# Kernel tuning notes

Measured on AMD Instinct MI355X. Metric: run time of the kernel, lower is better.

Reference implementation:

```python
import jax, jax.numpy as jnp
import numpy as np

C = 64
B, H, W = 4, 64, 64


def setup_inputs() -> dict:
    key = jax.random.key(0)
    ks = jax.random.split(key, 8)
    s = 0.05
    x = jax.random.normal(ks[0], (B, C, H, W), dtype=jnp.float32)
    Wq = jax.random.normal(ks[1], (C // 4, C), dtype=jnp.float32) * s
    bq = jax.random.normal(ks[2], (C // 4,), dtype=jnp.float32) * s
    Wk = jax.random.normal(ks[3], (C // 4, C), dtype=jnp.float32) * s
    bk = jax.random.normal(ks[4], (C // 4,), dtype=jnp.float32) * s
    Wv = jax.random.normal(ks[5], (C, C), dtype=jnp.float32) * s
    bv = jax.random.normal(ks[6], (C,), dtype=jnp.float32) * s
    gamma = jax.random.normal(ks[7], (1,), dtype=jnp.float32)
    return {"x": x, "Wq": Wq, "bq": bq, "Wk": Wk, "bk": bk, "Wv": Wv, "bv": bv, "gamma": gamma}


def reference(x, Wq, bq, Wk, bk, Wv, bv, gamma):
    b, c, h, w = x.shape
    n = h * w
    xf = x.reshape(b, c, n)  # [B, C, N]
    # 1x1 convs == channel GEMMs
    q = jnp.einsum('bcn,oc->bon', xf, Wq) + bq[None, :, None]  # [B, C/4, N]
    k = jnp.einsum('bcn,oc->bon', xf, Wk) + bk[None, :, None]  # [B, C/4, N]
    v = jnp.einsum('bcn,oc->bon', xf, Wv) + bv[None, :, None]  # [B, C, N]
    # attention[b, i, j] over key positions j (no 1/sqrt(d) scaling, per source)
    scores = jnp.einsum('bci,bcj->bij', q, k)  # [B, N, N]
    attn = jax.nn.softmax(scores, axis=-1)
    out = jnp.einsum('bcj,bij->bci', v, attn)  # [B, C, N]
    out = out.reshape(b, c, h, w)
    return gamma * out + x
```

## Files before the change

### kernel.cpp

```cpp
#include <hip/hip_runtime.h>

typedef short short8  __attribute__((ext_vector_type(8)));
typedef short short4v __attribute__((ext_vector_type(4)));
typedef float f32x4   __attribute__((ext_vector_type(4)));

static __device__ __forceinline__ unsigned short f2bf(float f) {
  unsigned int u = __builtin_bit_cast(unsigned int, f);
  u += 0x7fffu + ((u >> 16) & 1u);
  return (unsigned short)(u >> 16);
}
static __device__ __forceinline__ float bf2f(unsigned short u) {
  unsigned int v = ((unsigned int)u) << 16;
  return __builtin_bit_cast(float, v);
}
static __device__ __forceinline__ unsigned int pack2bf_rtz(float lo, float hi) {
  return __builtin_amdgcn_perm(__builtin_bit_cast(unsigned int, hi),
                               __builtin_bit_cast(unsigned int, lo), 0x07060302u);
}

__global__ __launch_bounds__(256) void qkv_mfma(
    const float* __restrict__ x,
    const float* __restrict__ Wq, const float* __restrict__ bq,
    const float* __restrict__ Wk, const float* __restrict__ bk,
    const float* __restrict__ Wv, const float* __restrict__ bv,
    unsigned short* __restrict__ qb, unsigned short* __restrict__ kb,
    unsigned short* __restrict__ vb)
{
  const int rt   = blockIdx.x;
  const int nt   = blockIdx.y;
  const int b    = blockIdx.z;
  const int lane = threadIdx.x & 63;
  const int wave = threadIdx.x >> 6;
  const int l15  = lane & 15;
  const int quad = lane >> 4;
  const int n    = nt * 64 + wave * 16 + l15;

  const float* wbase; const float* bias; int row0;
  if (rt == 0)      { wbase = Wq; bias = bq; row0 = 0; }
  else if (rt == 1) { wbase = Wk; bias = bk; row0 = 0; }
  else              { wbase = Wv; bias = bv; row0 = (rt - 2) * 16; }

  short8 bfrag[2];
#pragma unroll
  for (int ks = 0; ks < 2; ++ks)
#pragma unroll
    for (int jj = 0; jj < 8; ++jj) {
      const int c = ks * 32 + quad * 8 + jj;
      bfrag[ks][jj] = (short)f2bf(x[((size_t)(b * 64 + c)) * 4096 + n]);
    }

  short8 afrag[2];
#pragma unroll
  for (int ks = 0; ks < 2; ++ks) {
    f32x4 w0 = *(const f32x4*)(wbase + (row0 + l15) * 64 + ks * 32 + quad * 8);
    f32x4 w1 = *(const f32x4*)(wbase + (row0 + l15) * 64 + ks * 32 + quad * 8 + 4);
#pragma unroll
    for (int jj = 0; jj < 4; ++jj) {
      afrag[ks][jj]     = (short)f2bf(w0[jj]);
      afrag[ks][jj + 4] = (short)f2bf(w1[jj]);
    }
  }

  f32x4 acc;
#pragma unroll
  for (int r = 0; r < 4; ++r)
    acc[r] = bias[row0 + quad * 4 + r];
  acc = __builtin_amdgcn_mfma_f32_16x16x32_bf16(afrag[0], bfrag[0], acc, 0, 0, 0);
  acc = __builtin_amdgcn_mfma_f32_16x16x32_bf16(afrag[1], bfrag[1], acc, 0, 0, 0);

  if (rt <= 1) {
    if (rt == 0) {
#pragma unroll
      for (int r = 0; r < 4; ++r) acc[r] *= 1.44269504088896340736f;
    }
    short4v sv;
#pragma unroll
    for (int r = 0; r < 4; ++r) sv[r] = (short)f2bf(acc[r]);
    unsigned short* dst = (rt == 0 ? qb : kb);
    *(short4v*)(dst + (((size_t)b * 4096 + n) * 16) + quad * 4) = sv;
  } else {
#pragma unroll
    for (int r = 0; r < 4; ++r) {
      const int c = row0 + quad * 4 + r;
      vb[((size_t)(b * 64 + c)) * 4096 + n] = f2bf(acc[r]);
    }
  }
}

__global__ __launch_bounds__(512) void flash_fused(
    const unsigned short* __restrict__ qb, const unsigned short* __restrict__ kb,
    const unsigned short* __restrict__ vb,
    const float* __restrict__ x, const float* __restrict__ gptr,
    float* __restrict__ out)
{
  __shared__ unsigned short p_lds[8 * 4096];

  const int qg   = blockIdx.x;
  const int b    = blockIdx.y;
  const int t    = threadIdx.x;
  const int wave = t >> 6;
  const int lane = t & 63;
  const int l15  = lane & 15;
  const int quad = lane >> 4;
  const int sw   = l15 & 7;

  short8 qfrag[4];
#pragma unroll
  for (int qt = 0; qt < 4; ++qt) {
    qfrag[qt] = (short8)0;
    if (quad < 2) {
      const int iq = qg * 64 + qt * 16 + l15;
      qfrag[qt] = *(const short8*)(qb + (((size_t)b * 4096 + iq) * 16 + quad * 8));
    }
  }

  const unsigned short* vbb = vb + (size_t)b * 64 * 4096;
  const unsigned short* kbb = kb + (size_t)b * 4096 * 16;
  f32x4 acc[4][4];
#pragma unroll
  for (int qt = 0; qt < 4; ++qt)
#pragma unroll
    for (int ct = 0; ct < 4; ++ct) acc[qt][ct] = (f32x4)0.f;
  float lp[4] = {0.f, 0.f, 0.f, 0.f};
  unsigned short* pw = p_lds + wave * 4096;

  const int jbeg = wave * 512;
  const int jend = jbeg + 512;

  short8 kf[4];
#pragma unroll
  for (int sub = 0; sub < 4; ++sub) {
    kf[sub] = (short8)0;
    if (quad < 2)
      kf[sub] = *(const short8*)(kbb + (size_t)(jbeg + sub * 16 + l15) * 16 + quad * 8);
  }

#pragma unroll 1
  for (int j0 = jbeg; j0 < jend; j0 += 64) {
    short8 vf[2][4];
#pragma unroll
    for (int kc = 0; kc < 2; ++kc) {
      const int vcol = j0 + kc * 32 + quad * 8;
#pragma unroll
      for (int ct = 0; ct < 4; ++ct)
        vf[kc][ct] = *(const short8*)(vbb + (size_t)(ct * 16 + l15) * 4096 + vcol);
    }

#pragma unroll
    for (int qt = 0; qt < 4; ++qt) {
#pragma unroll
      for (int sub = 0; sub < 4; ++sub) {
        f32x4 sc = __builtin_amdgcn_mfma_f32_16x16x32_bf16(kf[sub], qfrag[qt], (f32x4)0.f, 0, 0, 0);
        float p0 = __builtin_amdgcn_exp2f(sc[0]);
        float p1 = __builtin_amdgcn_exp2f(sc[1]);
        float p2 = __builtin_amdgcn_exp2f(sc[2]);
        float p3 = __builtin_amdgcn_exp2f(sc[3]);
        lp[qt] += (p0 + p1) + (p2 + p3);
        const int ch = (sub * 2 + (quad >> 1)) ^ sw;
        unsigned int* dst = (unsigned int*)(pw + (qt * 16 + l15) * 64 + ch * 8 + (quad & 1) * 4);
        dst[0] = pack2bf_rtz(p0, p1);
        dst[1] = pack2bf_rtz(p2, p3);
      }
    }

    short8 kfn[4];
    const int jn = j0 + 64;
    const bool more = (jn < jend);
#pragma unroll
    for (int sub = 0; sub < 4; ++sub) {
      kfn[sub] = (short8)0;
      if (more && quad < 2)
        kfn[sub] = *(const short8*)(kbb + (size_t)(jn + sub * 16 + l15) * 16 + quad * 8);
    }

    __builtin_amdgcn_s_setprio(1);
#pragma unroll
    for (int kc = 0; kc < 2; ++kc) {
#pragma unroll
      for (int qt = 0; qt < 4; ++qt) {
        short8 pf = *(const short8*)(pw + (qt * 16 + l15) * 64 + ((kc * 4 + quad) ^ sw) * 8);
#pragma unroll
        for (int ct = 0; ct < 4; ++ct)
          acc[qt][ct] = __builtin_amdgcn_mfma_f32_16x16x32_bf16(vf[kc][ct], pf, acc[qt][ct], 0, 0, 0);
      }
    }
    __builtin_amdgcn_s_setprio(0);

#pragma unroll
    for (int sub = 0; sub < 4; ++sub) kf[sub] = kfn[sub];
  }

  float xr[8];
#pragma unroll
  for (int r = 0; r < 8; ++r) {
    const int c = wave * 8 + r;
    xr[r] = x[((size_t)(b * 64 + c)) * 4096 + (size_t)qg * 64 + lane];
  }

#pragma unroll
  for (int qt = 0; qt < 4; ++qt) {
    lp[qt] += __shfl_xor(lp[qt], 16);
    lp[qt] += __shfl_xor(lp[qt], 32);
  }

#pragma unroll
  for (int qt = 0; qt < 4; ++qt)
#pragma unroll
    for (int ct = 0; ct < 4; ++ct) {
      short4v sv;
#pragma unroll
      for (int r = 0; r < 4; ++r) sv[r] = (short)f2bf(acc[qt][ct][r]);
      const int q = qt * 16 + l15;
      const unsigned off = (unsigned)(q * 128 + (ct * 16 + quad * 4) * 2)
                         ^ (unsigned)((q & 7) << 4);
      *(short4v*)((char*)pw + off) = sv;
    }
  __syncthreads();

  float o[8] = {0.f, 0.f, 0.f, 0.f, 0.f, 0.f, 0.f, 0.f};
  const unsigned roff = (unsigned)(lane * 128 + wave * 16)
                      ^ (unsigned)((lane & 7) << 4);
#pragma unroll
  for (int w = 0; w < 8; ++w) {
    short8 v = *(const short8*)((const char*)(p_lds + w * 4096) + roff);
#pragma unroll
    for (int r = 0; r < 8; ++r) o[r] += bf2f((unsigned short)v[r]);
  }
  __syncthreads();

  float* lf = (float*)p_lds;
  if (lane < 16) {
#pragma unroll
    for (int qt = 0; qt < 4; ++qt)
      lf[wave * 64 + qt * 16 + lane] = lp[qt];
  }
  __syncthreads();
  float lsum = 0.f;
#pragma unroll
  for (int w = 0; w < 8; ++w) lsum += lf[w * 64 + lane];
  const float li = 1.f / lsum;
  const float g  = gptr[0];

#pragma unroll
  for (int r = 0; r < 8; ++r) {
    const int c = wave * 8 + r;
    const size_t off = ((size_t)(b * 64 + c)) * 4096 + (size_t)qg * 64 + lane;
    out[off] = g * (o[r] * li) + xr[r];
  }
}

extern "C" void kernel_launch(void* const* d_in, const int* in_sizes, int n_in,
                              void* d_out, int out_size, void* d_ws, size_t ws_size,
                              hipStream_t stream)
{
  const float* x  = (const float*)d_in[0];
  const float* Wq = (const float*)d_in[1];
  const float* bq = (const float*)d_in[2];
  const float* Wk = (const float*)d_in[3];
  const float* bk = (const float*)d_in[4];
  const float* Wv = (const float*)d_in[5];
  const float* bv = (const float*)d_in[6];
  const float* g  = (const float*)d_in[7];

  unsigned short* ws = (unsigned short*)d_ws;
  unsigned short* qb = ws;
  unsigned short* kb = ws + 262144;
  unsigned short* vb = ws + 524288;
  float* ob = (float*)d_out;

  hipLaunchKernelGGL(qkv_mfma, dim3(6, 64, 4), dim3(256), 0, stream,
                     x, Wq, bq, Wk, bk, Wv, bv, qb, kb, vb);
  hipLaunchKernelGGL(flash_fused, dim3(64, 4), dim3(512), 0, stream,
                     qb, kb, vb, x, g, ob);
}
```

Baseline: 96.07 us.

## Fuse QKV projection into attention kernel with cooperative grid sync

Merges the QKV projection kernel and the flash attention kernel into one cooperative launch. Each block computes Q for its own query tile straight into LDS, plus its share of K and V for global memory, then runs a grid-wide sync before the attention phase. This removes one kernel launch and the global round trip for Q. In exchange it adds a grid barrier and requires all 256 blocks of 512 threads with 64KB LDS to be co-resident, and the cooperative launch path may carry its own overhead.

```diff
diff --git a/kernel.cpp b/kernel.cpp
--- a/kernel.cpp
+++ b/kernel.cpp
@@ -1,4 +1,7 @@
 #include <hip/hip_runtime.h>
+#include <hip/hip_cooperative_groups.h>
+
+namespace cg = cooperative_groups;
 
 typedef short short8  __attribute__((ext_vector_type(8)));
 typedef short short4v __attribute__((ext_vector_type(4)));
@@ -18,83 +21,15 @@
                                __builtin_bit_cast(unsigned int, lo), 0x07060302u);
 }
 
-__global__ __launch_bounds__(256) void qkv_mfma(
+__global__ __launch_bounds__(512) void fused_all(
     const float* __restrict__ x,
     const float* __restrict__ Wq, const float* __restrict__ bq,
     const float* __restrict__ Wk, const float* __restrict__ bk,
     const float* __restrict__ Wv, const float* __restrict__ bv,
-    unsigned short* __restrict__ qb, unsigned short* __restrict__ kb,
-    unsigned short* __restrict__ vb)
-{
-  const int rt   = blockIdx.x;
-  const int nt   = blockIdx.y;
-  const int b    = blockIdx.z;
-  const int lane = threadIdx.x & 63;
-  const int wave = threadIdx.x >> 6;
-  const int l15  = lane & 15;
-  const int quad = lane >> 4;
-  const int n    = nt * 64 + wave * 16 + l15;
-
-  const float* wbase; const float* bias; int row0;
-  if (rt == 0)      { wbase = Wq; bias = bq; row0 = 0; }
-  else if (rt == 1) { wbase = Wk; bias = bk; row0 = 0; }
-  else              { wbase = Wv; bias = bv; row0 = (rt - 2) * 16; }
-
-  short8 bfrag[2];
-#pragma unroll
-  for (int ks = 0; ks < 2; ++ks)
-#pragma unroll
-    for (int jj = 0; jj < 8; ++jj) {
-      const int c = ks * 32 + quad * 8 + jj;
-      bfrag[ks][jj] = (short)f2bf(x[((size_t)(b * 64 + c)) * 4096 + n]);
-    }
-
-  short8 afrag[2];
-#pragma unroll
-  for (int ks = 0; ks < 2; ++ks) {
-    f32x4 w0 = *(const f32x4*)(wbase + (row0 + l15) * 64 + ks * 32 + quad * 8);
-    f32x4 w1 = *(const f32x4*)(wbase + (row0 + l15) * 64 + ks * 32 + quad * 8 + 4);
-#pragma unroll
-    for (int jj = 0; jj < 4; ++jj) {
-      afrag[ks][jj]     = (short)f2bf(w0[jj]);
-      afrag[ks][jj + 4] = (short)f2bf(w1[jj]);
-    }
-  }
-
-  f32x4 acc;
-#pragma unroll
-  for (int r = 0; r < 4; ++r)
-    acc[r] = bias[row0 + quad * 4 + r];
-  acc = __builtin_amdgcn_mfma_f32_16x16x32_bf16(afrag[0], bfrag[0], acc, 0, 0, 0);
-  acc = __builtin_amdgcn_mfma_f32_16x16x32_bf16(afrag[1], bfrag[1], acc, 0, 0, 0);
-
-  if (rt <= 1) {
-    if (rt == 0) {
-#pragma unroll
-      for (int r = 0; r < 4; ++r) acc[r] *= 1.44269504088896340736f;
-    }
-    short4v sv;
-#pragma unroll
-    for (int r = 0; r < 4; ++r) sv[r] = (short)f2bf(acc[r]);
-    unsigned short* dst = (rt == 0 ? qb : kb);
-    *(short4v*)(dst + (((size_t)b * 4096 + n) * 16) + quad * 4) = sv;
-  } else {
-#pragma unroll
-    for (int r = 0; r < 4; ++r) {
-      const int c = row0 + quad * 4 + r;
-      vb[((size_t)(b * 64 + c)) * 4096 + n] = f2bf(acc[r]);
-    }
-  }
-}
-
-__global__ __launch_bounds__(512) void flash_fused(
-    const unsigned short* __restrict__ qb, const unsigned short* __restrict__ kb,
-    const unsigned short* __restrict__ vb,
-    const float* __restrict__ x, const float* __restrict__ gptr,
-    float* __restrict__ out)
+    unsigned short* __restrict__ kb, unsigned short* __restrict__ vb,
+    const float* __restrict__ gptr, float* __restrict__ out)
 {
   __shared__ unsigned short p_lds[8 * 4096];
-
   const int qg   = blockIdx.x;
   const int b    = blockIdx.y;
   const int t    = threadIdx.x;
@@ -104,15 +39,80 @@
   const int quad = lane >> 4;
   const int sw   = l15 & 7;
 
+  {
+    const int slice = wave & 3;
+    const int n     = qg * 64 + slice * 16 + l15;
+
+    short8 bfrag[2];
+#pragma unroll
+    for (int ks = 0; ks < 2; ++ks)
+#pragma unroll
+      for (int jj = 0; jj < 8; ++jj) {
+        const int c = ks * 32 + quad * 8 + jj;
+        bfrag[ks][jj] = (short)f2bf(x[((size_t)(b * 64 + c)) * 4096 + n]);
+      }
+
+#pragma unroll
+    for (int rr = 0; rr < 3; ++rr) {
+      const int rt = (wave >> 2) + rr * 2;
+      const float* wbase; const float* bias; int row0;
+      if (rt == 0)      { wbase = Wq; bias = bq; row0 = 0; }
+      else if (rt == 1) { wbase = Wk; bias = bk; row0 = 0; }
+      else              { wbase = Wv; bias = bv; row0 = (rt - 2) * 16; }
+
+      short8 afrag[2];
+#pragma unroll
+      for (int ks = 0; ks < 2; ++ks) {
+        f32x4 w0 = *(const f32x4*)(wbase + (row0 + l15) * 64 + ks * 32 + quad * 8);
+        f32x4 w1 = *(const f32x4*)(wbase + (row0 + l15) * 64 + ks * 32 + quad * 8 + 4);
+#pragma unroll
+        for (int jj = 0; jj < 4; ++jj) {
+          afrag[ks][jj]     = (short)f2bf(w0[jj]);
+          afrag[ks][jj + 4] = (short)f2bf(w1[jj]);
+        }
+      }
+
+      f32x4 acc;
+#pragma unroll
+      for (int r = 0; r < 4; ++r)
+        acc[r] = bias[row0 + quad * 4 + r];
+      acc = __builtin_amdgcn_mfma_f32_16x16x32_bf16(afrag[0], bfrag[0], acc, 0, 0, 0);
+      acc = __builtin_amdgcn_mfma_f32_16x16x32_bf16(afrag[1], bfrag[1], acc, 0, 0, 0);
+
+      if (rt == 0) {
+#pragma unroll
+        for (int r = 0; r < 4; ++r) acc[r] *= 1.44269504088896340736f;
+        short4v sv;
+#pragma unroll
+        for (int r = 0; r < 4; ++r) sv[r] = (short)f2bf(acc[r]);
+        *(short4v*)(p_lds + (slice * 16 + l15) * 16 + quad * 4) = sv;
+      } else if (rt == 1) {
+        short4v sv;
+#pragma unroll
+        for (int r = 0; r < 4; ++r) sv[r] = (short)f2bf(acc[r]);
+        *(short4v*)(kb + (((size_t)b * 4096 + n) * 16) + quad * 4) = sv;
+      } else {
+#pragma unroll
+        for (int r = 0; r < 4; ++r) {
+          const int c = row0 + quad * 4 + r;
+          vb[((size_t)(b * 64 + c)) * 4096 + n] = f2bf(acc[r]);
+        }
+      }
+    }
+  }
+  __syncthreads();
+
   short8 qfrag[4];
 #pragma unroll
   for (int qt = 0; qt < 4; ++qt) {
     qfrag[qt] = (short8)0;
-    if (quad < 2) {
-      const int iq = qg * 64 + qt * 16 + l15;
-      qfrag[qt] = *(const short8*)(qb + (((size_t)b * 4096 + iq) * 16 + quad * 8));
-    }
-  }
+    if (quad < 2)
+      qfrag[qt] = *(const short8*)(p_lds + (qt * 16 + l15) * 16 + quad * 8);
+  }
+
+  __threadfence();
+  cg::this_grid().sync();
+  __threadfence();
 
   const unsigned short* vbb = vb + (size_t)b * 64 * 4096;
   const unsigned short* kbb = kb + (size_t)b * 4096 * 16;
@@ -263,13 +263,14 @@
   const float* g  = (const float*)d_in[7];
 
   unsigned short* ws = (unsigned short*)d_ws;
-  unsigned short* qb = ws;
-  unsigned short* kb = ws + 262144;
-  unsigned short* vb = ws + 524288;
+  unsigned short* kb = ws;
+  unsigned short* vb = ws + 262144;
   float* ob = (float*)d_out;
 
-  hipLaunchKernelGGL(qkv_mfma, dim3(6, 64, 4), dim3(256), 0, stream,
-                     x, Wq, bq, Wk, bk, Wv, bv, qb, kb, vb);
-  hipLaunchKernelGGL(flash_fused, dim3(64, 4), dim3(512), 0, stream,
-                     qb, kb, vb, x, g, ob);
-}
+  void* args[] = {
+    (void*)&x, (void*)&Wq, (void*)&bq, (void*)&Wk, (void*)&bk,
+    (void*)&Wv, (void*)&bv, (void*)&kb, (void*)&vb, (void*)&g, (void*)&ob
+  };
+  hipLaunchCooperativeKernel((const void*)fused_all, dim3(64, 4), dim3(512),
+                             args, 0, stream);
+}
```

New measurement: 184.2 us. 91.7% more time.
